# Kernel tuning notes

Hardware: AMD Instinct MI355X
Metric: run time of the kernel (lower is better)

The kernel has to match this reference:

```python
import jax, jax.numpy as jnp
import numpy as np
import math

D_MODEL = 1024
N_HEADS = 16


def setup_inputs() -> dict:
    key = jax.random.key(0)
    ks = jax.random.split(key, 11)
    N, L, S = 2, 2048, 2048
    d = D_MODEL
    s = 1.0 / math.sqrt(d)
    return {
        "queries": jax.random.normal(ks[0], (N, L, d), dtype=jnp.float32),
        "keys": jax.random.normal(ks[1], (N, S, d), dtype=jnp.float32),
        "values": jax.random.normal(ks[2], (N, S, d), dtype=jnp.float32),
        # torch nn.Linear weights are [out_features, in_features]
        "Wq": jax.random.normal(ks[3], (d, d), dtype=jnp.float32) * s,
        "bq": jax.random.normal(ks[4], (d,), dtype=jnp.float32) * s,
        "Wk": jax.random.normal(ks[5], (d, d), dtype=jnp.float32) * s,
        "bk": jax.random.normal(ks[6], (d,), dtype=jnp.float32) * s,
        "Wv": jax.random.normal(ks[7], (d, d), dtype=jnp.float32) * s,
        "bv": jax.random.normal(ks[8], (d,), dtype=jnp.float32) * s,
        "Wo": jax.random.normal(ks[9], (d, d), dtype=jnp.float32) * s,
        "bo": jax.random.normal(ks[10], (d,), dtype=jnp.float32) * s,
    }


def reference(queries, keys, values, Wq, bq, Wk, bk, Wv, bv, Wo, bo):
    N, L, _ = queries.shape
    S = keys.shape[1]
    H = N_HEADS
    # projections (torch Linear: x @ W.T + b), reshape to heads
    q = (queries @ Wq.T + bq).reshape(N, L, H, -1)
    k = (keys @ Wk.T + bk).reshape(N, S, H, -1)
    v = (values @ Wv.T + bv).reshape(N, S, H, -1)
    D = k.shape[-1]
    # full attention score map [N, L, H, S]
    sm = jnp.einsum('nlhd,nshd->nlhs', q, k) / math.sqrt(D)
    # causal mask: position l attends to s <= l
    causal_mask = jnp.triu(jnp.ones((L, S), dtype=bool), k=1)  # True = masked
    sm = jnp.where(causal_mask[None, :, None, :], -jnp.inf, sm)
    sm = jax.nn.softmax(sm, axis=-1)
    attn = jnp.einsum('nlhs,nshd->nlhd', sm, v)  # [N, L, H, D]
    new_values = attn.reshape(N, L, H * D)
    return new_values @ Wo.T + bo
```

## Files before the change

kernel.cpp:

```cpp
#include <hip/hip_runtime.h>

typedef unsigned short u16;
typedef unsigned int u32;
typedef __attribute__((ext_vector_type(8))) short bf16x8;
typedef __attribute__((ext_vector_type(4))) float f32x4;
typedef __attribute__((ext_vector_type(16))) float f32x16;
typedef __attribute__((ext_vector_type(4))) float floatx4;
typedef __attribute__((ext_vector_type(4))) u16 u16x4;

__device__ __forceinline__ u16 f2bf(float x) {
  union { float f; u32 u; } c; c.f = x;
  return (u16)((c.u + 0x7fffu + ((c.u >> 16) & 1u)) >> 16);
}
__device__ __forceinline__ u32 packbf(float a, float b) {
  return (u32)f2bf(a) | ((u32)f2bf(b) << 16);
}
__device__ __forceinline__ u32 cvtpk(float lo, float hi) {
  u32 r;
  asm("v_cvt_pk_bf16_f32 %0, %1, %2" : "=v"(r) : "v"(lo), "v"(hi));
  return r;
}
__device__ __forceinline__ float bf2f(u16 v) {
  union { u32 u; float f; } c; c.u = (u32)v << 16; return c.f;
}

__device__ __forceinline__ void gload16(const u16* g, u16* l) {
  auto gp = (const __attribute__((address_space(1))) unsigned int*)g;
  auto lp = (__attribute__((address_space(3))) unsigned int*)l;
  __builtin_amdgcn_global_load_lds(gp, lp, 16, 0, 0);
}

__global__ void cvt7(const float* s0, const float* s1, const float* s2,
                     const float* s3, const float* s4, const float* s5, const float* s6,
                     u16* d0, u16* d1, u16* d2, u16* d3, u16* d4, u16* d5, u16* d6) {
  const int y = blockIdx.y;
  const float* s = (y == 0) ? s0 : (y == 1) ? s1 : (y == 2) ? s2 : (y == 3) ? s3
                  : (y == 4) ? s4 : (y == 5) ? s5 : s6;
  u16* d = (y == 0) ? d0 : (y == 1) ? d1 : (y == 2) ? d2 : (y == 3) ? d3
          : (y == 4) ? d4 : (y == 5) ? d5 : d6;
  const int n4 = (y < 3) ? (1 << 20) : (1 << 18);
  int i = blockIdx.x * 256 + threadIdx.x;
  if (i < n4) {
    floatx4 v = ((const floatx4*)s)[i];
    u16x4 o;
    o.x = f2bf(v.x); o.y = f2bf(v.y); o.z = f2bf(v.z); o.w = f2bf(v.w);
    ((u16x4*)d)[i] = o;
  }
}

__global__ __launch_bounds__(256) void gemm3(const u16* A0, const u16* A1, const u16* A2,
                                             const u16* W0, const u16* W1, const u16* W2,
                                             const float* b0, const float* b1, const float* b2,
                                             u16* o0, u16* o1, u16* o2) {
  __shared__ u16 lA[128 * 32];
  __shared__ u16 lB[128 * 32];
  const int z = blockIdx.z;
  const u16* A  = (z == 0) ? A0 : (z == 1) ? A1 : A2;
  const u16* Bw = (z == 0) ? W0 : (z == 1) ? W1 : W2;
  const float* bias = (z == 0) ? b0 : (z == 1) ? b1 : b2;
  u16* outp = (z == 0) ? o0 : (z == 1) ? o1 : o2;
  const float scl = (z == 0) ? (0.125f * 1.44269504089f) : 1.0f;

  const int tid = threadIdx.x;
  const int brow = blockIdx.y * 128, bcol = blockIdx.x * 128;
  const int lane = tid & 63, w = tid >> 6;
  const int wr = w >> 1, wc = w & 1;
  const int fr = lane & 15, fq = lane >> 4;
  f32x4 acc[4][4] = {};

  for (int k0 = 0; k0 < 1024; k0 += 32) {
    __syncthreads();
#pragma unroll
    for (int it = 0; it < 2; ++it) {
      int chunk = tid + it * 256;
      int row = chunk >> 2;
      int col = (chunk & 3) * 8;
      gload16(A  + (size_t)(brow + row) * 1024 + k0 + col, &lA[chunk * 8]);
      gload16(Bw + (size_t)(bcol + row) * 1024 + k0 + col, &lB[chunk * 8]);
    }
    __syncthreads();
    bf16x8 af[4], bfr[4];
#pragma unroll
    for (int m = 0; m < 4; ++m) af[m]  = *(const bf16x8*)&lA[(wr * 64 + m * 16 + fr) * 32 + fq * 8];
#pragma unroll
    for (int n = 0; n < 4; ++n) bfr[n] = *(const bf16x8*)&lB[(wc * 64 + n * 16 + fr) * 32 + fq * 8];
#pragma unroll
    for (int m = 0; m < 4; ++m)
#pragma unroll
      for (int n = 0; n < 4; ++n)
        acc[m][n] = __builtin_amdgcn_mfma_f32_16x16x32_bf16(af[m], bfr[n], acc[m][n], 0, 0, 0);
  }

#pragma unroll
  for (int m = 0; m < 4; ++m) {
#pragma unroll
    for (int n = 0; n < 4; ++n) {
      int colg = bcol + wc * 64 + n * 16 + fr;
      float bv = bias[colg];
#pragma unroll
      for (int j = 0; j < 4; ++j) {
        int rowg = brow + wr * 64 + m * 16 + fq * 4 + j;
        float v = (acc[m][n][j] + bv) * scl;
        int nb = rowg >> 11, l = rowg & 2047;
        int h = colg >> 6, dd = colg & 63;
        size_t idx = (z < 2) ? (((size_t)(nb * 16 + h) * 2048 + l) * 64 + dd)
                             : (((size_t)(nb * 16 + h) * 64 + dd) * 2048 + l);
        outp[idx] = f2bf(v);
      }
    }
  }
}

__global__ __launch_bounds__(256) void gemm_o(const u16* __restrict__ A,
                                              const u16* __restrict__ Bw,
                                              const float* __restrict__ bias,
                                              float* __restrict__ outp) {
  __shared__ u16 lA[128 * 32];
  __shared__ u16 lB[128 * 32];
  const int tid = threadIdx.x;
  const int brow = blockIdx.y * 128, bcol = blockIdx.x * 128;
  const int lane = tid & 63, w = tid >> 6;
  const int wr = w >> 1, wc = w & 1;
  const int fr = lane & 15, fq = lane >> 4;
  f32x4 acc[4][4] = {};

  for (int k0 = 0; k0 < 1024; k0 += 32) {
    __syncthreads();
#pragma unroll
    for (int it = 0; it < 2; ++it) {
      int chunk = tid + it * 256;
      int row = chunk >> 2;
      int col = (chunk & 3) * 8;
      gload16(A  + (size_t)(brow + row) * 1024 + k0 + col, &lA[chunk * 8]);
      gload16(Bw + (size_t)(bcol + row) * 1024 + k0 + col, &lB[chunk * 8]);
    }
    __syncthreads();
    bf16x8 af[4], bfr[4];
#pragma unroll
    for (int m = 0; m < 4; ++m) af[m]  = *(const bf16x8*)&lA[(wr * 64 + m * 16 + fr) * 32 + fq * 8];
#pragma unroll
    for (int n = 0; n < 4; ++n) bfr[n] = *(const bf16x8*)&lB[(wc * 64 + n * 16 + fr) * 32 + fq * 8];
#pragma unroll
    for (int m = 0; m < 4; ++m)
#pragma unroll
      for (int n = 0; n < 4; ++n)
        acc[m][n] = __builtin_amdgcn_mfma_f32_16x16x32_bf16(af[m], bfr[n], acc[m][n], 0, 0, 0);
  }

#pragma unroll
  for (int m = 0; m < 4; ++m) {
#pragma unroll
    for (int n = 0; n < 4; ++n) {
      int colg = bcol + wc * 64 + n * 16 + fr;
      float bv = bias[colg];
#pragma unroll
      for (int j = 0; j < 4; ++j) {
        int rowg = brow + wr * 64 + m * 16 + fq * 4 + j;
        outp[(size_t)rowg * 1024 + colg] = acc[m][n][j] + bv;
      }
    }
  }
}

__global__ __launch_bounds__(256) void attn_part(const u16* __restrict__ Qp,
                                                 const u16* __restrict__ Kp,
                                                 const u16* __restrict__ Vt,
                                                 u16* __restrict__ accP,
                                                 float* __restrict__ mP,
                                                 float* __restrict__ lP) {
  const int lane = threadIdx.x & 63, w = threadIdx.x >> 6;
  const int wid = blockIdx.x * 4 + w;
  const int nh = wid / 160;
  const int j = wid - nh * 160;
  int p, t;
  if (j < 64)       { p = 0; t = j; }
  else if (j < 112) { p = 1; t = 16 + (j - 64); }
  else if (j < 144) { p = 2; t = 32 + (j - 112); }
  else              { p = 3; t = 48 + (j - 144); }
  const int q0 = t * 32;
  const int col = lane & 31, hi = lane >> 5;
  const u16* Q = Qp + (size_t)nh * 2048 * 64;
  const u16* K = Kp + (size_t)nh * 2048 * 64;
  const u16* V = Vt + (size_t)nh * 64 * 2048;
  const int q = q0 + col;

  bf16x8 qf[4];
#pragma unroll
  for (int ks = 0; ks < 4; ++ks) qf[ks] = *(const bf16x8*)&Q[(size_t)q * 64 + ks * 16 + hi * 8];

  const int i0 = p * 16;
  const int i1 = min(i0 + 16, t + 1);

  f32x16 acc0 = {}, acc1 = {};
  float mrow = -1e30f, lrow = 0.f;

  for (int i = i0; i < i1; ++i) {
    const int s0 = i * 32;
    f32x16 sc = {};
    __builtin_amdgcn_s_setprio(1);
#pragma unroll
    for (int ks = 0; ks < 4; ++ks) {
      bf16x8 kf = *(const bf16x8*)&K[(size_t)(s0 + col) * 64 + ks * 16 + hi * 8];
      sc = __builtin_amdgcn_mfma_f32_32x32x16_bf16(kf, qf[ks], sc, 0, 0, 0);
    }
    __builtin_amdgcn_s_setprio(0);
    float pr[16];
    float pmax = -1e30f;
    const bool diag = (i == t);
#pragma unroll
    for (int r = 0; r < 16; ++r) {
      int sr = (r & 3) + 8 * (r >> 2) + 4 * hi;
      float v = sc[r];
      if (diag && sr > col) v = -1e30f;
      pr[r] = v;
      pmax = fmaxf(pmax, v);
    }
    pmax = fmaxf(pmax, __shfl_xor(pmax, 32));
    if (!__all(pmax <= mrow + 8.f)) {
      float mnew = fmaxf(mrow, pmax);
      float alpha = exp2f(mrow - mnew);
#pragma unroll
      for (int r = 0; r < 16; ++r) { acc0[r] *= alpha; acc1[r] *= alpha; }
      lrow *= alpha;
      mrow = mnew;
    }
    float ps = 0.f;
#pragma unroll
    for (int r = 0; r < 16; ++r) { float pv = exp2f(pr[r] - mrow); pr[r] = pv; ps += pv; }
    ps += __shfl_xor(ps, 32);
    lrow += ps;

#pragma unroll
    for (int ks = 0; ks < 2; ++ks) {
      u32 A0 = cvtpk(pr[8 * ks + 0], pr[8 * ks + 1]);
      u32 A1 = cvtpk(pr[8 * ks + 2], pr[8 * ks + 3]);
      u32 B0 = cvtpk(pr[8 * ks + 4], pr[8 * ks + 5]);
      u32 B1 = cvtpk(pr[8 * ks + 6], pr[8 * ks + 7]);
      u32 t0 = __shfl_xor(hi ? A0 : B0, 32);
      u32 t1 = __shfl_xor(hi ? A1 : B1, 32);
      union { u32 u[4]; bf16x8 v; } pf;
      pf.u[0] = hi ? t0 : A0;
      pf.u[1] = hi ? t1 : A1;
      pf.u[2] = hi ? B0 : t0;
      pf.u[3] = hi ? B1 : t1;
      bf16x8 vf0 = *(const bf16x8*)&V[(size_t)(col) * 2048 + s0 + ks * 16 + hi * 8];
      bf16x8 vf1 = *(const bf16x8*)&V[(size_t)(32 + col) * 2048 + s0 + ks * 16 + hi * 8];
      __builtin_amdgcn_s_setprio(1);
      acc0 = __builtin_amdgcn_mfma_f32_32x32x16_bf16(vf0, pf.v, acc0, 0, 0, 0);
      acc1 = __builtin_amdgcn_mfma_f32_32x32x16_bf16(vf1, pf.v, acc1, 0, 0, 0);
      __builtin_amdgcn_s_setprio(0);
    }
  }

  u16* base = accP + (size_t)wid * 2048 + col * 64;
#pragma unroll
  for (int rp = 0; rp < 8; ++rp) {
    int r = rp * 2;
    int d = (r & 3) + 8 * (r >> 2) + 4 * hi;
    *(u32*)&base[d]      = packbf(acc0[r], acc0[r + 1]);
    *(u32*)&base[32 + d] = packbf(acc1[r], acc1[r + 1]);
  }
  if (hi == 0) {
    mP[wid * 32 + col] = mrow;
    lP[wid * 32 + col] = lrow;
  }
}

__global__ void combineN(const u16* __restrict__ accP, const float* __restrict__ mP,
                         const float* __restrict__ lP, u16* __restrict__ at) {
  const int t = blockIdx.x;
  const int nh = blockIdx.y;
  const int q = threadIdx.x >> 3;
  const int d0 = (threadIdx.x & 7) * 8;
  const int np = (t >> 4) + 1;
  const int s0 = nh * 160 + t;
  const int s1 = nh * 160 + 64 + (t - 16);
  const int s2 = nh * 160 + 112 + (t - 32);
  const int s3 = nh * 160 + 144 + (t - 48);

  float m = mP[s0 * 32 + q];
  if (np > 1) m = fmaxf(m, mP[s1 * 32 + q]);
  if (np > 2) m = fmaxf(m, mP[s2 * 32 + q]);
  if (np > 3) m = fmaxf(m, mP[s3 * 32 + q]);
  float w0 = exp2f(mP[s0 * 32 + q] - m);
  float w1 = (np > 1) ? exp2f(mP[s1 * 32 + q] - m) : 0.f;
  float w2 = (np > 2) ? exp2f(mP[s2 * 32 + q] - m) : 0.f;
  float w3 = (np > 3) ? exp2f(mP[s3 * 32 + q] - m) : 0.f;
  float l = lP[s0 * 32 + q] * w0;
  if (np > 1) l += lP[s1 * 32 + q] * w1;
  if (np > 2) l += lP[s2 * 32 + q] * w2;
  if (np > 3) l += lP[s3 * 32 + q] * w3;
  const float inv = 1.f / l;
  w0 *= inv; w1 *= inv; w2 *= inv; w3 *= inv;

  float o[8] = {};
  {
    const bf16x8 a = *(const bf16x8*)&accP[(size_t)s0 * 2048 + q * 64 + d0];
#pragma unroll
    for (int k = 0; k < 8; ++k) o[k] += bf2f((u16)a[k]) * w0;
  }
  if (np > 1) {
    const bf16x8 a = *(const bf16x8*)&accP[(size_t)s1 * 2048 + q * 64 + d0];
#pragma unroll
    for (int k = 0; k < 8; ++k) o[k] += bf2f((u16)a[k]) * w1;
  }
  if (np > 2) {
    const bf16x8 a = *(const bf16x8*)&accP[(size_t)s2 * 2048 + q * 64 + d0];
#pragma unroll
    for (int k = 0; k < 8; ++k) o[k] += bf2f((u16)a[k]) * w2;
  }
  if (np > 3) {
    const bf16x8 a = *(const bf16x8*)&accP[(size_t)s3 * 2048 + q * 64 + d0];
#pragma unroll
    for (int k = 0; k < 8; ++k) o[k] += bf2f((u16)a[k]) * w3;
  }

  const int nb = nh >> 4, h = nh & 15;
  u16* op = &at[((size_t)(nb * 2048 + t * 32 + q)) * 1024 + h * 64 + d0];
#pragma unroll
  for (int jj = 0; jj < 4; ++jj)
    *(u32*)&op[2 * jj] = packbf(o[2 * jj], o[2 * jj + 1]);
}

extern "C" void kernel_launch(void* const* d_in, const int* in_sizes, int n_in,
                              void* d_out, int out_size, void* d_ws, size_t ws_size,
                              hipStream_t stream) {
  const float* queries = (const float*)d_in[0];
  const float* keys    = (const float*)d_in[1];
  const float* values  = (const float*)d_in[2];
  const float* Wq = (const float*)d_in[3]; const float* bq = (const float*)d_in[4];
  const float* Wk = (const float*)d_in[5]; const float* bk = (const float*)d_in[6];
  const float* Wv = (const float*)d_in[7]; const float* bv = (const float*)d_in[8];
  const float* Wo = (const float*)d_in[9]; const float* bo = (const float*)d_in[10];
  float* out = (float*)d_out;
  char* ws = (char*)d_ws;

  const size_t MB = 1u << 20;
  u16* xq  = (u16*)(ws + 0 * MB);
  u16* xk  = (u16*)(ws + 8 * MB);
  u16* xv  = (u16*)(ws + 16 * MB);
  u16* wqb = (u16*)(ws + 24 * MB);
  u16* wkb = (u16*)(ws + 26 * MB);
  u16* wvb = (u16*)(ws + 28 * MB);
  u16* wob = (u16*)(ws + 30 * MB);
  u16* qp  = (u16*)(ws + 32 * MB);
  u16* kp  = (u16*)(ws + 40 * MB);
  u16* vt  = (u16*)(ws + 48 * MB);
  u16* at  = xq;
  u16*   accP = (u16*)(ws + 8 * MB);
  float* mPp  = (float*)(ws + 28 * MB);
  float* lPp  = (float*)(ws + 28 * MB + 5120 * 32 * sizeof(float));

  cvt7<<<dim3(4096, 7), 256, 0, stream>>>(queries, keys, values, Wq, Wk, Wv, Wo,
                                          xq, xk, xv, wqb, wkb, wvb, wob);
  gemm3<<<dim3(8, 32, 3), 256, 0, stream>>>(xq, xk, xv, wqb, wkb, wvb,
                                            bq, bk, bv, qp, kp, vt);
  attn_part<<<1280, 256, 0, stream>>>(qp, kp, vt, accP, mPp, lPp);
  combineN<<<dim3(64, 32), 256, 0, stream>>>(accP, mPp, lPp, at);
  gemm_o<<<dim3(8, 32), 256, 0, stream>>>(at, wob, bo, out);
}
```

Baseline: 284.1 us.

## Share K/V tiles across four waves via double-buffered swizzled LDS in attention

Each attention block now owns 128 queries (four waves of 32) instead of each wave working alone. K and V tiles are staged once per block into double-buffered, XOR-swizzled shared memory using gload16 prefetch, so four waves reuse each tile rather than each reading it from global memory. The causal mask is now computed per element from absolute positions, because a tile can be partially masked for some waves. The split-KV partition and the combine indexing are rescaled to match. This adds a __syncthreads per K-tile and gives coarser, less balanced causal work per block.

```diff
diff --git a/kernel.cpp b/kernel.cpp
--- a/kernel.cpp
+++ b/kernel.cpp
@@ -168,50 +168,68 @@
                                                  u16* __restrict__ accP,
                                                  float* __restrict__ mP,
                                                  float* __restrict__ lP) {
-  const int lane = threadIdx.x & 63, w = threadIdx.x >> 6;
-  const int wid = blockIdx.x * 4 + w;
-  const int nh = wid / 160;
-  const int j = wid - nh * 160;
+  __shared__ u16 lK[2][2048];
+  __shared__ u16 lV[2][2048];
+  const int tid = threadIdx.x;
+  const int lane = tid & 63, w = tid >> 6;
+  const int bid = blockIdx.x;
+  const int nh = bid / 40;
+  const int j = bid - nh * 40;
   int p, t;
-  if (j < 64)       { p = 0; t = j; }
-  else if (j < 112) { p = 1; t = 16 + (j - 64); }
-  else if (j < 144) { p = 2; t = 32 + (j - 112); }
-  else              { p = 3; t = 48 + (j - 144); }
-  const int q0 = t * 32;
+  if (j < 16)      { p = 0; t = j; }
+  else if (j < 28) { p = 1; t = 4 + (j - 16); }
+  else if (j < 36) { p = 2; t = 8 + (j - 28); }
+  else             { p = 3; t = 12 + (j - 36); }
+  const int i0 = p * 16;
+  const int i1 = min(i0 + 16, (t + 1) * 4);
   const int col = lane & 31, hi = lane >> 5;
   const u16* Q = Qp + (size_t)nh * 2048 * 64;
   const u16* K = Kp + (size_t)nh * 2048 * 64;
   const u16* V = Vt + (size_t)nh * 64 * 2048;
-  const int q = q0 + col;
+  const int q = t * 128 + w * 32 + col;
+  const int swz = (col & 7) << 4;
+
+  const int kr  = tid >> 3;
+  const int kin = ((tid & 7) * 16) ^ ((kr & 7) << 4);
+  const int vd  = kr + ((kin >> 6) << 5);
+  const int vs  = (kin & 63) >> 1;
 
   bf16x8 qf[4];
 #pragma unroll
   for (int ks = 0; ks < 4; ++ks) qf[ks] = *(const bf16x8*)&Q[(size_t)q * 64 + ks * 16 + hi * 8];
-
-  const int i0 = p * 16;
-  const int i1 = min(i0 + 16, t + 1);
 
   f32x16 acc0 = {}, acc1 = {};
   float mrow = -1e30f, lrow = 0.f;
 
+  {
+    const int s0 = i0 * 32;
+    gload16(K + (size_t)(s0 + kr) * 64 + (kin >> 1), &lK[0][tid * 8]);
+    gload16(V + (size_t)vd * 2048 + (s0 + vs),       &lV[0][tid * 8]);
+  }
+  __syncthreads();
+
+  int cur = 0;
   for (int i = i0; i < i1; ++i) {
+    if (i + 1 < i1) {
+      const int s0n = (i + 1) * 32;
+      gload16(K + (size_t)(s0n + kr) * 64 + (kin >> 1), &lK[cur ^ 1][tid * 8]);
+      gload16(V + (size_t)vd * 2048 + (s0n + vs),       &lV[cur ^ 1][tid * 8]);
+    }
     const int s0 = i * 32;
     f32x16 sc = {};
     __builtin_amdgcn_s_setprio(1);
 #pragma unroll
     for (int ks = 0; ks < 4; ++ks) {
-      bf16x8 kf = *(const bf16x8*)&K[(size_t)(s0 + col) * 64 + ks * 16 + hi * 8];
+      bf16x8 kf = *(const bf16x8*)&lK[cur][col * 64 + (((ks * 32 + hi * 16) ^ swz) >> 1)];
       sc = __builtin_amdgcn_mfma_f32_32x32x16_bf16(kf, qf[ks], sc, 0, 0, 0);
     }
     __builtin_amdgcn_s_setprio(0);
     float pr[16];
     float pmax = -1e30f;
-    const bool diag = (i == t);
 #pragma unroll
     for (int r = 0; r < 16; ++r) {
       int sr = (r & 3) + 8 * (r >> 2) + 4 * hi;
-      float v = sc[r];
-      if (diag && sr > col) v = -1e30f;
+      float v = (s0 + sr > q) ? -1e30f : sc[r];
       pr[r] = v;
       pmax = fmaxf(pmax, v);
     }
@@ -243,16 +261,19 @@
       pf.u[1] = hi ? t1 : A1;
       pf.u[2] = hi ? B0 : t0;
       pf.u[3] = hi ? B1 : t1;
-      bf16x8 vf0 = *(const bf16x8*)&V[(size_t)(col) * 2048 + s0 + ks * 16 + hi * 8];
-      bf16x8 vf1 = *(const bf16x8*)&V[(size_t)(32 + col) * 2048 + s0 + ks * 16 + hi * 8];
+      bf16x8 vf0 = *(const bf16x8*)&lV[cur][col * 64 + (((ks * 32 + hi * 16) ^ swz) >> 1)];
+      bf16x8 vf1 = *(const bf16x8*)&lV[cur][col * 64 + (((64 + ks * 32 + hi * 16) ^ swz) >> 1)];
       __builtin_amdgcn_s_setprio(1);
       acc0 = __builtin_amdgcn_mfma_f32_32x32x16_bf16(vf0, pf.v, acc0, 0, 0, 0);
       acc1 = __builtin_amdgcn_mfma_f32_32x32x16_bf16(vf1, pf.v, acc1, 0, 0, 0);
       __builtin_amdgcn_s_setprio(0);
     }
-  }
-
-  u16* base = accP + (size_t)wid * 2048 + col * 64;
+    __syncthreads();
+    cur ^= 1;
+  }
+
+  const int ql = w * 32 + col;
+  u16* base = accP + (size_t)bid * 8192 + ql * 64;
 #pragma unroll
   for (int rp = 0; rp < 8; ++rp) {
     int r = rp * 2;
@@ -261,62 +282,63 @@
     *(u32*)&base[32 + d] = packbf(acc1[r], acc1[r + 1]);
   }
   if (hi == 0) {
-    mP[wid * 32 + col] = mrow;
-    lP[wid * 32 + col] = lrow;
+    mP[bid * 128 + ql] = mrow;
+    lP[bid * 128 + ql] = lrow;
   }
 }
 
 __global__ void combineN(const u16* __restrict__ accP, const float* __restrict__ mP,
                          const float* __restrict__ lP, u16* __restrict__ at) {
-  const int t = blockIdx.x;
+  const int t = blockIdx.x >> 2;
+  const int seg = blockIdx.x & 3;
   const int nh = blockIdx.y;
-  const int q = threadIdx.x >> 3;
+  const int ql = seg * 32 + (threadIdx.x >> 3);
   const int d0 = (threadIdx.x & 7) * 8;
-  const int np = (t >> 4) + 1;
-  const int s0 = nh * 160 + t;
-  const int s1 = nh * 160 + 64 + (t - 16);
-  const int s2 = nh * 160 + 112 + (t - 32);
-  const int s3 = nh * 160 + 144 + (t - 48);
-
-  float m = mP[s0 * 32 + q];
-  if (np > 1) m = fmaxf(m, mP[s1 * 32 + q]);
-  if (np > 2) m = fmaxf(m, mP[s2 * 32 + q]);
-  if (np > 3) m = fmaxf(m, mP[s3 * 32 + q]);
-  float w0 = exp2f(mP[s0 * 32 + q] - m);
-  float w1 = (np > 1) ? exp2f(mP[s1 * 32 + q] - m) : 0.f;
-  float w2 = (np > 2) ? exp2f(mP[s2 * 32 + q] - m) : 0.f;
-  float w3 = (np > 3) ? exp2f(mP[s3 * 32 + q] - m) : 0.f;
-  float l = lP[s0 * 32 + q] * w0;
-  if (np > 1) l += lP[s1 * 32 + q] * w1;
-  if (np > 2) l += lP[s2 * 32 + q] * w2;
-  if (np > 3) l += lP[s3 * 32 + q] * w3;
+  const int np = (t >> 2) + 1;
+  const int s0 = nh * 40 + t;
+  const int s1 = nh * 40 + 16 + (t - 4);
+  const int s2 = nh * 40 + 28 + (t - 8);
+  const int s3 = nh * 40 + 36 + (t - 12);
+
+  float m = mP[s0 * 128 + ql];
+  if (np > 1) m = fmaxf(m, mP[s1 * 128 + ql]);
+  if (np > 2) m = fmaxf(m, mP[s2 * 128 + ql]);
+  if (np > 3) m = fmaxf(m, mP[s3 * 128 + ql]);
+  float w0 = exp2f(mP[s0 * 128 + ql] - m);
+  float w1 = (np > 1) ? exp2f(mP[s1 * 128 + ql] - m) : 0.f;
+  float w2 = (np > 2) ? exp2f(mP[s2 * 128 + ql] - m) : 0.f;
+  float w3 = (np > 3) ? exp2f(mP[s3 * 128 + ql] - m) : 0.f;
+  float l = lP[s0 * 128 + ql] * w0;
+  if (np > 1) l += lP[s1 * 128 + ql] * w1;
+  if (np > 2) l += lP[s2 * 128 + ql] * w2;
+  if (np > 3) l += lP[s3 * 128 + ql] * w3;
   const float inv = 1.f / l;
   w0 *= inv; w1 *= inv; w2 *= inv; w3 *= inv;
 
   float o[8] = {};
   {
-    const bf16x8 a = *(const bf16x8*)&accP[(size_t)s0 * 2048 + q * 64 + d0];
+    const bf16x8 a = *(const bf16x8*)&accP[(size_t)s0 * 8192 + ql * 64 + d0];
 #pragma unroll
     for (int k = 0; k < 8; ++k) o[k] += bf2f((u16)a[k]) * w0;
   }
   if (np > 1) {
-    const bf16x8 a = *(const bf16x8*)&accP[(size_t)s1 * 2048 + q * 64 + d0];
+    const bf16x8 a = *(const bf16x8*)&accP[(size_t)s1 * 8192 + ql * 64 + d0];
 #pragma unroll
     for (int k = 0; k < 8; ++k) o[k] += bf2f((u16)a[k]) * w1;
   }
   if (np > 2) {
-    const bf16x8 a = *(const bf16x8*)&accP[(size_t)s2 * 2048 + q * 64 + d0];
+    const bf16x8 a = *(const bf16x8*)&accP[(size_t)s2 * 8192 + ql * 64 + d0];
 #pragma unroll
     for (int k = 0; k < 8; ++k) o[k] += bf2f((u16)a[k]) * w2;
   }
   if (np > 3) {
-    const bf16x8 a = *(const bf16x8*)&accP[(size_t)s3 * 2048 + q * 64 + d0];
+    const bf16x8 a = *(const bf16x8*)&accP[(size_t)s3 * 8192 + ql * 64 + d0];
 #pragma unroll
     for (int k = 0; k < 8; ++k) o[k] += bf2f((u16)a[k]) * w3;
   }
 
   const int nb = nh >> 4, h = nh & 15;
-  u16* op = &at[((size_t)(nb * 2048 + t * 32 + q)) * 1024 + h * 64 + d0];
+  u16* op = &at[((size_t)(nb * 2048 + t * 128 + ql)) * 1024 + h * 64 + d0];
 #pragma unroll
   for (int jj = 0; jj < 4; ++jj)
     *(u32*)&op[2 * jj] = packbf(o[2 * jj], o[2 * jj + 1]);
@@ -349,7 +371,7 @@
   u16* at  = xq;
   u16*   accP = (u16*)(ws + 8 * MB);
   float* mPp  = (float*)(ws + 28 * MB);
-  float* lPp  = (float*)(ws + 28 * MB + 5120 * 32 * sizeof(float));
+  float* lPp  = (float*)(ws + 28 * MB + 1280 * 128 * sizeof(float));
 
   cvt7<<<dim3(4096, 7), 256, 0, stream>>>(queries, keys, values, Wq, Wk, Wv, Wo,
                                           xq, xk, xv, wqb, wkb, wvb, wob);
```

Result: faster. 249.7 us (-12.1%).
